# Optimization experiments

Hardware: AMD Instinct MI355X
Metric: run time of the kernel (lower is better)

## Reference

```python
import jax, jax.numpy as jnp
from jax import lax
import numpy as np

NINP, NHID, T, B = 512, 1024, 512, 64


def setup_inputs() -> dict:
    key = jax.random.key(0)
    ks = jax.random.split(key, 16)
    si = 1.0 / np.sqrt(NINP)
    sh = 1.0 / np.sqrt(NHID)
    inp = {
        "input": jax.random.normal(ks[0], (T, B, NINP), dtype=jnp.float32),
        "h": jax.random.normal(ks[1], (1, B, NHID), dtype=jnp.float32),
        "Wiz_w": jax.random.uniform(ks[2], (NHID, NINP), jnp.float32, -si, si),
        "Wiz_b": jax.random.uniform(ks[3], (NHID,), jnp.float32, -si, si),
        "Wir_w": jax.random.uniform(ks[4], (NHID, NINP), jnp.float32, -si, si),
        "Wir_b": jax.random.uniform(ks[5], (NHID,), jnp.float32, -si, si),
        "Wih_w": jax.random.uniform(ks[6], (NHID, NINP), jnp.float32, -si, si),
        "Wih_b": jax.random.uniform(ks[7], (NHID,), jnp.float32, -si, si),
        "Whz_w": jax.random.uniform(ks[8], (NHID, NHID), jnp.float32, -sh, sh),
        "Whz_b": jax.random.uniform(ks[9], (NHID,), jnp.float32, -sh, sh),
        "Whr_w": jax.random.uniform(ks[10], (NHID, NHID), jnp.float32, -sh, sh),
        "Whr_b": jax.random.uniform(ks[11], (NHID,), jnp.float32, -sh, sh),
        "Whh_w": jax.random.uniform(ks[12], (NHID, NHID), jnp.float32, -sh, sh),
        "Whh_b": jax.random.uniform(ks[13], (NHID,), jnp.float32, -sh, sh),
    }
    lengths = jax.random.randint(ks[14], (B,), 1, T + 1)
    lengths = lengths.at[0].set(T)  # ensure max_length == T (static scan length)
    inp["lengths"] = lengths.astype(jnp.int64)
    return inp


def reference(input, h, Wiz_w, Wiz_b, Wir_w, Wir_b, Wih_w, Wih_b,
              Whz_w, Whz_b, Whr_w, Whr_b, Whh_w, Whh_b, lengths):
    h0 = h[0]  # squeeze(0): [B, nhid]
    # Precompute input projections for all timesteps in one batched GEMM each: [T, B, nhid]
    xz = jnp.einsum('tbi,hi->tbh', input, Wiz_w) + Wiz_b
    xr = jnp.einsum('tbi,hi->tbh', input, Wir_w) + Wir_b
    xh = jnp.einsum('tbi,hi->tbh', input, Wih_w) + Wih_b
    tsteps = jnp.arange(input.shape[0])

    def step(hprev, inputs):
        xz_t, xr_t, xh_t, t = inputs
        z = jax.nn.sigmoid(hprev @ Whz_w.T + Whz_b + xz_t)
        r = jax.nn.sigmoid(hprev @ Whr_w.T + Whr_b + xr_t)
        h_cand = jnp.tanh((r * hprev) @ Whh_w.T + Whh_b + xh_t)
        h_new = (1.0 - z) * hprev + z * h_cand
        mask = (t < lengths).astype(hprev.dtype)[:, None]  # [B, 1]
        hn = h_new * mask + hprev * (1.0 - mask)
        return hn, hn

    h_last, hidden_stacked = lax.scan(step, h0, (xz, xr, xh, tsteps))
    return hidden_stacked, h_last[None]  # ([T,B,nhid], [1,B,nhid])
```

## Files before the change

### kernel.cpp

```cpp
#include <hip/hip_runtime.h>

typedef unsigned int   uint;
typedef unsigned short ushort;

#define NINP    512
#define NHID    1024
#define T_STEPS 512
#define B_SZ    64
#define KTOT    1536
#define BN      (B_SZ * NHID)

typedef __attribute__((ext_vector_type(8))) short bf16x8;
typedef __attribute__((ext_vector_type(4))) float f32x4;
typedef __attribute__((ext_vector_type(4))) uint  uintx4;

#define WCOMB_BYTES (3 * NHID * KTOT * 2)
#define WS_BSUM     (WCOMB_BYTES)
#define WS_HP       (WS_BSUM + 3 * NHID * 4)
#define WS_RHP      (WS_HP + BN * 4)
#define WS_BAR      (WS_RHP + BN * 4)
#define WS_NEED     (WS_BAR + 65536)

#define FH_OFF  8192

__device__ __forceinline__ float sigmoidf_(float x) { return 1.0f / (1.0f + __expf(-x)); }
__device__ __forceinline__ float tanhf_(float x)    { return 1.0f - 2.0f / (__expf(2.0f * x) + 1.0f); }

__device__ __forceinline__ ushort bf16_rne(float f) {
    uint u = __float_as_uint(f);
    return (ushort)((u + 0x7FFFu + ((u >> 16) & 1u)) >> 16);
}
__device__ __forceinline__ float bf16_to_f(ushort s) { return __uint_as_float(((uint)s) << 16); }
__device__ __forceinline__ bf16x8 ld8(const ushort* p) { return *(const bf16x8*)p; }
__device__ __forceinline__ bf16x8 cvt8(const float* p) {
    float4 a = *(const float4*)p;
    float4 b = *(const float4*)(p + 4);
    bf16x8 r;
    r[0] = (short)bf16_rne(a.x); r[1] = (short)bf16_rne(a.y);
    r[2] = (short)bf16_rne(a.z); r[3] = (short)bf16_rne(a.w);
    r[4] = (short)bf16_rne(b.x); r[5] = (short)bf16_rne(b.y);
    r[6] = (short)bf16_rne(b.z); r[7] = (short)bf16_rne(b.w);
    return r;
}
__device__ __forceinline__ f32x4 zero4() { f32x4 z = {0.f, 0.f, 0.f, 0.f}; return z; }
#define MFMA(a, b, c) __builtin_amdgcn_mfma_f32_16x16x32_bf16((a), (b), (c), 0, 0, 0)

__device__ __forceinline__ uint ld_rlx(uint* p) {
    return __hip_atomic_load(p, __ATOMIC_RELAXED, __HIP_MEMORY_SCOPE_AGENT);
}
__device__ __forceinline__ void st_rlx(uint* p, uint v) {
    __hip_atomic_store(p, v, __ATOMIC_RELAXED, __HIP_MEMORY_SCOPE_AGENT);
}
__device__ __forceinline__ void ld_state(const uint* p, uintx4& a, uintx4& b) {
    asm volatile("global_load_dwordx4 %0, %1, off sc0 sc1"
                 : "=v"(a) : "v"(p) : "memory");
    asm volatile("global_load_dwordx4 %0, %1, off offset:16 sc0 sc1"
                 : "=v"(b) : "v"(p) : "memory");
}
__device__ __forceinline__ void poll_ge(const uint* p, uint target) {
    for (;;) {
        uint v;
        asm volatile("global_load_dword %0, %1, off sc0 sc1\n\t"
                     "s_waitcnt vmcnt(0)"
                     : "=v"(v) : "v"(p) : "memory");
        if (__all(v >= target)) break;
        __builtin_amdgcn_s_sleep(1);
    }
}
__device__ __forceinline__ bf16x8 hi_frag(uintx4 a, uintx4 b) {
    uintx4 r;
    r[0] = __builtin_amdgcn_perm(a[1], a[0], 0x05040100u);
    r[1] = __builtin_amdgcn_perm(a[3], a[2], 0x05040100u);
    r[2] = __builtin_amdgcn_perm(b[1], b[0], 0x05040100u);
    r[3] = __builtin_amdgcn_perm(b[3], b[2], 0x05040100u);
    return *(bf16x8*)&r;
}
__device__ __forceinline__ bf16x8 lo_frag(uintx4 a, uintx4 b) {
    uintx4 r;
    r[0] = __builtin_amdgcn_perm(a[1], a[0], 0x07060302u);
    r[1] = __builtin_amdgcn_perm(a[3], a[2], 0x07060302u);
    r[2] = __builtin_amdgcn_perm(b[1], b[0], 0x07060302u);
    r[3] = __builtin_amdgcn_perm(b[3], b[2], 0x07060302u);
    return *(bf16x8*)&r;
}
__device__ __forceinline__ uint pack_hl(float v) {
    ushort hi = bf16_rne(v);
    ushort lo = bf16_rne(v - bf16_to_f(hi));
    return (uint)hi | ((uint)lo << 16);
}

__global__ __launch_bounds__(256) void prep_w(
    const float* __restrict__ Wiz, const float* __restrict__ Wir, const float* __restrict__ Wih,
    const float* __restrict__ Whz, const float* __restrict__ Whr, const float* __restrict__ Whh,
    ushort* __restrict__ wcomb)
{
    int tid = blockIdx.x * 256 + threadIdx.x;
    int oct = tid % (KTOT / 8);
    int row = tid / (KTOT / 8);
    int gate = row >> 10, n = row & 1023;
    int k0 = oct * 8;
    const float* src; int off;
    if (k0 < NINP) { src = gate == 0 ? Wiz : (gate == 1 ? Wir : Wih); off = n * NINP + k0; }
    else           { src = gate == 0 ? Whz : (gate == 1 ? Whr : Whh); off = n * NHID + (k0 - NINP); }
    ushort* dst = wcomb + (size_t)row * KTOT + k0;
    #pragma unroll
    for (int j = 0; j < 8; ++j) dst[j] = bf16_rne(src[off + j]);
}

__global__ __launch_bounds__(256) void prep_misc(
    const float* __restrict__ h0,
    const float* __restrict__ biz, const float* __restrict__ bir, const float* __restrict__ bih,
    const float* __restrict__ bhz, const float* __restrict__ bhr, const float* __restrict__ bhh,
    uint* __restrict__ hp, float* __restrict__ bsum, uint* __restrict__ bar)
{
    if (blockIdx.x < 256) {
        int i = blockIdx.x * 256 + threadIdx.x;
        hp[i] = pack_hl(h0[i]);
    } else {
        for (int n = threadIdx.x; n < NHID; n += 256) {
            bsum[n]            = biz[n] + bhz[n];
            bsum[NHID + n]     = bir[n] + bhr[n];
            bsum[2 * NHID + n] = bih[n] + bhh[n];
        }
        for (int i = threadIdx.x; i < 16384; i += 256) bar[i] = 0u;
    }
}

__global__ __launch_bounds__(512, 1) void gru_persist(
    const float* __restrict__ x, const float* __restrict__ h0,
    const void* __restrict__ lengths_raw,
    const ushort* __restrict__ wcomb, const float* __restrict__ bsum,
    uint* __restrict__ hp, uint* __restrict__ rhp,
    uint* __restrict__ bar, float* __restrict__ out)
{
    const int bid = blockIdx.x;
    const int nt = bid >> 2, mt = bid & 3;
    const int nbase = nt * 16, mbase = mt * 16;
    const int tid = threadIdx.x;
    const int wv = tid >> 6, lane = tid & 63;
    const int col = lane & 15, quad = lane >> 4;
    const int q8 = quad * 8;

    __shared__ f32x4 lds_acc1[2][8][2][64];
    __shared__ f32x4 lds_acc2[8][64];
    __shared__ uint  lds_pad[11264];
    lds_pad[tid & 1023] = tid;

    const int pslot = lane & 7;
    const int prod  = 2 * wv + 16 * (pslot >> 1) + (pslot & 1);
    uint* fr_ptr = bar + ((size_t)(mt * 64 + prod)) * 32;
    uint* fh_ptr = bar + FH_OFF + ((size_t)(mt * 64 + prod)) * 32;
    uint* my_fr  = bar + ((size_t)(mt * 64 + nt)) * 32;
    uint* my_fh  = bar + FH_OFF + ((size_t)(mt * 64 + nt)) * 32;

    bf16x8 wfz[6], wfr[6], wfc[6];
    #pragma unroll
    for (int s = 0; s < 6; ++s) {
        const int j = wv + 8 * s;
        const size_t ko = (size_t)j * 32 + q8;
        wfz[s] = ld8(wcomb + (size_t)(0 * NHID + nbase + col) * KTOT + ko);
        wfr[s] = ld8(wcomb + (size_t)(1 * NHID + nbase + col) * KTOT + ko);
        wfc[s] = ld8(wcomb + (size_t)(2 * NHID + nbase + col) * KTOT + ko);
    }

    const int* l32 = (const int*)lengths_raw;
    const bool is64 = (l32[1] == 0);
    int len[4];
    float h_reg[4];
    #pragma unroll
    for (int i = 0; i < 4; ++i) {
        const int b = mbase + quad * 4 + i;
        len[i]   = is64 ? (int)((const long long*)lengths_raw)[b] : l32[b];
        h_reg[i] = h0[(size_t)b * NHID + nbase + col];
    }

    const float bias_z = bsum[nbase + col];
    const float bias_r = bsum[NHID + nbase + col];
    const float bias_c = bsum[2 * NHID + nbase + col];

    const size_t arow = (size_t)(mbase + col);

    const uint* hpp[4]; const uint* rpp[4]; size_t gi4[4];
    #pragma unroll
    for (int s = 0; s < 4; ++s) {
        const int kh = (wv + 8 * (s + 2)) * 32 - NINP;
        hpp[s] = hp  + arow * NHID + kh + q8;
        rpp[s] = rhp + arow * NHID + kh + q8;
    }
    #pragma unroll
    for (int i = 0; i < 4; ++i)
        gi4[i] = (size_t)(mbase + quad * 4 + i) * NHID + nbase + col;

    f32x4 zsig = zero4();
    bf16x8 xf[2];

    f32x4 az = zero4(), ar = zero4();
    #pragma unroll
    for (int s = 0; s < 2; ++s) {
        const int k = (wv + 8 * s) * 32;
        xf[s] = cvt8(x + arow * NINP + k + q8);
        az = MFMA(xf[s], wfz[s], az);
        ar = MFMA(xf[s], wfr[s], ar);
    }

    for (int t = 0; t < T_STEPS; ++t) {
        const int par = t & 1;
        if (t) poll_ge(fh_ptr, (uint)t);
        {
            uintx4 qa[4], qb[4];
            #pragma unroll
            for (int s = 0; s < 4; ++s) ld_state(hpp[s], qa[s], qb[s]);
            asm volatile("s_waitcnt vmcnt(0)" ::: "memory");
            __builtin_amdgcn_sched_barrier(0);
            #pragma unroll
            for (int s = 0; s < 4; ++s) {
                const bf16x8 hi = hi_frag(qa[s], qb[s]);
                const bf16x8 lo = lo_frag(qa[s], qb[s]);
                az = MFMA(hi, wfz[s + 2], az);
                ar = MFMA(hi, wfr[s + 2], ar);
                az = MFMA(lo, wfz[s + 2], az);
                ar = MFMA(lo, wfr[s + 2], ar);
            }
        }
        lds_acc1[par][wv][0][lane] = az;
        lds_acc1[par][wv][1][lane] = ar;
        __syncthreads();
        if (wv == 0) {
            f32x4 rp = {bias_r, bias_r, bias_r, bias_r};
            #pragma unroll
            for (int w = 0; w < 8; ++w) {
                const f32x4 a = lds_acc1[par][w][1][lane];
                #pragma unroll
                for (int i = 0; i < 4; ++i) rp[i] += a[i];
            }
            #pragma unroll
            for (int i = 0; i < 4; ++i)
                st_rlx(&rhp[gi4[i]], pack_hl(sigmoidf_(rp[i]) * h_reg[i]));
            asm volatile("s_waitcnt vmcnt(0)" ::: "memory");
            if (lane == 0) st_rlx(my_fr, (uint)(t + 1));
        }
        if (wv < 2) {
            f32x4 zp = {bias_z, bias_z, bias_z, bias_z};
            #pragma unroll
            for (int w = 0; w < 8; ++w) {
                const f32x4 a = lds_acc1[par][w][0][lane];
                #pragma unroll
                for (int i = 0; i < 4; ++i) zp[i] += a[i];
            }
            #pragma unroll
            for (int i = 0; i < 4; ++i) zsig[i] = sigmoidf_(zp[i]);
        }
        f32x4 ac = zero4();
        ac = MFMA(xf[0], wfc[0], ac);
        ac = MFMA(xf[1], wfc[1], ac);

        poll_ge(fr_ptr, (uint)(t + 1));
        {
            uintx4 qa[4], qb[4];
            #pragma unroll
            for (int s = 0; s < 4; ++s) ld_state(rpp[s], qa[s], qb[s]);
            asm volatile("s_waitcnt vmcnt(0)" ::: "memory");
            __builtin_amdgcn_sched_barrier(0);
            #pragma unroll
            for (int s = 0; s < 4; ++s) {
                const bf16x8 hi = hi_frag(qa[s], qb[s]);
                const bf16x8 lo = lo_frag(qa[s], qb[s]);
                ac = MFMA(hi, wfc[s + 2], ac);
                ac = MFMA(lo, wfc[s + 2], ac);
            }
        }
        lds_acc2[wv][lane] = ac;
        __syncthreads();
        if (wv < 2) {
            f32x4 cp = {bias_c, bias_c, bias_c, bias_c};
            #pragma unroll
            for (int w = 0; w < 8; ++w) {
                const f32x4 a = lds_acc2[w][lane];
                #pragma unroll
                for (int i = 0; i < 4; ++i) cp[i] += a[i];
            }
            float hn4[4];
            #pragma unroll
            for (int i = 0; i < 4; ++i) {
                const float c = tanhf_(cp[i]);
                const float h = h_reg[i];
                hn4[i] = (t < len[i]) ? fmaf(zsig[i], c - h, h) : h;
                h_reg[i] = hn4[i];
            }
            if (wv == 1) {
                #pragma unroll
                for (int i = 0; i < 4; ++i) st_rlx(&hp[gi4[i]], pack_hl(hn4[i]));
                asm volatile("s_waitcnt vmcnt(0)" ::: "memory");
                if (lane == 0) st_rlx(my_fh, (uint)(t + 1));
            } else {
                float* out_t = out + (size_t)t * BN;
                #pragma unroll
                for (int i = 0; i < 4; ++i) {
                    __builtin_nontemporal_store(hn4[i], &out_t[gi4[i]]);
                    if (t == T_STEPS - 1)
                        __builtin_nontemporal_store(hn4[i], &out[(size_t)T_STEPS * BN + gi4[i]]);
                }
            }
        }
        az = zero4(); ar = zero4();
        if (t + 1 < T_STEPS) {
            const float* x_t = x + (size_t)(t + 1) * B_SZ * NINP;
            #pragma unroll
            for (int s = 0; s < 2; ++s) {
                const int k = (wv + 8 * s) * 32;
                xf[s] = cvt8(x_t + arow * NINP + k + q8);
                az = MFMA(xf[s], wfz[s], az);
                ar = MFMA(xf[s], wfr[s], ar);
            }
        }
    }

    if (ld_rlx(&bar[1023]) == 0xDEADBEEFu)
        out[0] = (float)lds_pad[tid & 1023];
}

__global__ void gru_ws_probe_mb(float* p) {
    if (blockIdx.x == 0xFFFFFFFFu) p[0] = 0.f;
}

extern "C" void kernel_launch(void* const* d_in, const int* in_sizes, int n_in,
                              void* d_out, int out_size, void* d_ws, size_t ws_size,
                              hipStream_t stream) {
    const float* x   = (const float*)d_in[0];
    const float* h0  = (const float*)d_in[1];
    const float* Wiz = (const float*)d_in[2];  const float* biz = (const float*)d_in[3];
    const float* Wir = (const float*)d_in[4];  const float* bir = (const float*)d_in[5];
    const float* Wih = (const float*)d_in[6];  const float* bih = (const float*)d_in[7];
    const float* Whz = (const float*)d_in[8];  const float* bhz = (const float*)d_in[9];
    const float* Whr = (const float*)d_in[10]; const float* bhr = (const float*)d_in[11];
    const float* Whh = (const float*)d_in[12]; const float* bhh = (const float*)d_in[13];
    const void*  lengths = d_in[14];
    float* out = (float*)d_out;
    char*  ws  = (char*)d_ws;

    size_t mb = ws_size >> 20; if (mb > 2048) mb = 2048;
    gru_ws_probe_mb<<<dim3((uint)mb + 1), 64, 0, stream>>>((float*)d_ws);
    if (ws_size < (size_t)WS_NEED) return;

    ushort* wcomb = (ushort*)ws;
    float*  bsum  = (float*)(ws + WS_BSUM);
    uint*   hp    = (uint*)(ws + WS_HP);
    uint*   rhp   = (uint*)(ws + WS_RHP);
    uint*   bar   = (uint*)(ws + WS_BAR);

    prep_w<<<2304, 256, 0, stream>>>(Wiz, Wir, Wih, Whz, Whr, Whh, wcomb);
    prep_misc<<<257, 256, 0, stream>>>(h0, biz, bir, bih, bhz, bhr, bhh, hp, bsum, bar);
    gru_persist<<<256, 512, 0, stream>>>(x, h0, lengths, wcomb, bsum,
                                         hp, rhp, bar, out);
}
```

Before: 4.141 ms.

## Replace flag barriers with per-element tagged state words polled directly

Drops the separate producer flag arrays and polling. Each hidden-state and r*h element is now stored as a 64-bit word holding the packed value plus a timestep tag, and consumers spin on the data loads until every tag reaches the target step. This removes the flag round trip (store data, wait, store flag, then poll flag, then load data). The epilogue is also spread over four waves, one batch row each, instead of two waves handling four rows. The cost is twice the state traffic per poll and repeated full-data reloads while spinning. Correctness depends on each 64-bit store being seen atomically.

```diff
diff --git a/kernel.cpp b/kernel.cpp
--- a/kernel.cpp
+++ b/kernel.cpp
@@ -1,7 +1,8 @@
 #include <hip/hip_runtime.h>
 
-typedef unsigned int   uint;
-typedef unsigned short ushort;
+typedef unsigned int       uint;
+typedef unsigned short     ushort;
+typedef unsigned long long ull;
 
 #define NINP    512
 #define NHID    1024
@@ -16,12 +17,9 @@
 
 #define WCOMB_BYTES (3 * NHID * KTOT * 2)
 #define WS_BSUM     (WCOMB_BYTES)
-#define WS_HP       (WS_BSUM + 3 * NHID * 4)
-#define WS_RHP      (WS_HP + BN * 4)
-#define WS_BAR      (WS_RHP + BN * 4)
-#define WS_NEED     (WS_BAR + 65536)
-
-#define FH_OFF  8192
+#define WS_HP2      (WS_BSUM + 3 * NHID * 4)
+#define WS_RHP2     (WS_HP2 + BN * 8)
+#define WS_NEED     (WS_RHP2 + BN * 8)
 
 __device__ __forceinline__ float sigmoidf_(float x) { return 1.0f / (1.0f + __expf(-x)); }
 __device__ __forceinline__ float tanhf_(float x)    { return 1.0f - 2.0f / (__expf(2.0f * x) + 1.0f); }
@@ -45,48 +43,69 @@
 __device__ __forceinline__ f32x4 zero4() { f32x4 z = {0.f, 0.f, 0.f, 0.f}; return z; }
 #define MFMA(a, b, c) __builtin_amdgcn_mfma_f32_16x16x32_bf16((a), (b), (c), 0, 0, 0)
 
-__device__ __forceinline__ uint ld_rlx(uint* p) {
+__device__ __forceinline__ uint ld_rlx(const uint* p) {
     return __hip_atomic_load(p, __ATOMIC_RELAXED, __HIP_MEMORY_SCOPE_AGENT);
 }
-__device__ __forceinline__ void st_rlx(uint* p, uint v) {
+__device__ __forceinline__ void st_state(ull* p, uint val, uint tag) {
+    ull v = (ull)val | ((ull)tag << 32);
     __hip_atomic_store(p, v, __ATOMIC_RELAXED, __HIP_MEMORY_SCOPE_AGENT);
-}
-__device__ __forceinline__ void ld_state(const uint* p, uintx4& a, uintx4& b) {
-    asm volatile("global_load_dwordx4 %0, %1, off sc0 sc1"
-                 : "=v"(a) : "v"(p) : "memory");
-    asm volatile("global_load_dwordx4 %0, %1, off offset:16 sc0 sc1"
-                 : "=v"(b) : "v"(p) : "memory");
-}
-__device__ __forceinline__ void poll_ge(const uint* p, uint target) {
-    for (;;) {
-        uint v;
-        asm volatile("global_load_dword %0, %1, off sc0 sc1\n\t"
-                     "s_waitcnt vmcnt(0)"
-                     : "=v"(v) : "v"(p) : "memory");
-        if (__all(v >= target)) break;
-        __builtin_amdgcn_s_sleep(1);
-    }
-}
-__device__ __forceinline__ bf16x8 hi_frag(uintx4 a, uintx4 b) {
-    uintx4 r;
-    r[0] = __builtin_amdgcn_perm(a[1], a[0], 0x05040100u);
-    r[1] = __builtin_amdgcn_perm(a[3], a[2], 0x05040100u);
-    r[2] = __builtin_amdgcn_perm(b[1], b[0], 0x05040100u);
-    r[3] = __builtin_amdgcn_perm(b[3], b[2], 0x05040100u);
-    return *(bf16x8*)&r;
-}
-__device__ __forceinline__ bf16x8 lo_frag(uintx4 a, uintx4 b) {
-    uintx4 r;
-    r[0] = __builtin_amdgcn_perm(a[1], a[0], 0x07060302u);
-    r[1] = __builtin_amdgcn_perm(a[3], a[2], 0x07060302u);
-    r[2] = __builtin_amdgcn_perm(b[1], b[0], 0x07060302u);
-    r[3] = __builtin_amdgcn_perm(b[3], b[2], 0x07060302u);
-    return *(bf16x8*)&r;
 }
 __device__ __forceinline__ uint pack_hl(float v) {
     ushort hi = bf16_rne(v);
     ushort lo = bf16_rne(v - bf16_to_f(hi));
     return (uint)hi | ((uint)lo << 16);
+}
+
+__device__ __forceinline__ void poll_load(const ull* b, uint target, uintx4 q[4][4]) {
+    const uint* p0 = (const uint*)b;
+    const uint* p1 = (const uint*)(b + 512);
+    for (;;) {
+        asm volatile("global_load_dwordx4 %0, %1, off sc0 sc1"             : "=v"(q[0][0]) : "v"(p0) : "memory");
+        asm volatile("global_load_dwordx4 %0, %1, off offset:16 sc0 sc1"   : "=v"(q[0][1]) : "v"(p0) : "memory");
+        asm volatile("global_load_dwordx4 %0, %1, off offset:32 sc0 sc1"   : "=v"(q[0][2]) : "v"(p0) : "memory");
+        asm volatile("global_load_dwordx4 %0, %1, off offset:48 sc0 sc1"   : "=v"(q[0][3]) : "v"(p0) : "memory");
+        asm volatile("global_load_dwordx4 %0, %1, off offset:2048 sc0 sc1" : "=v"(q[1][0]) : "v"(p0) : "memory");
+        asm volatile("global_load_dwordx4 %0, %1, off offset:2064 sc0 sc1" : "=v"(q[1][1]) : "v"(p0) : "memory");
+        asm volatile("global_load_dwordx4 %0, %1, off offset:2080 sc0 sc1" : "=v"(q[1][2]) : "v"(p0) : "memory");
+        asm volatile("global_load_dwordx4 %0, %1, off offset:2096 sc0 sc1" : "=v"(q[1][3]) : "v"(p0) : "memory");
+        asm volatile("global_load_dwordx4 %0, %1, off sc0 sc1"             : "=v"(q[2][0]) : "v"(p1) : "memory");
+        asm volatile("global_load_dwordx4 %0, %1, off offset:16 sc0 sc1"   : "=v"(q[2][1]) : "v"(p1) : "memory");
+        asm volatile("global_load_dwordx4 %0, %1, off offset:32 sc0 sc1"   : "=v"(q[2][2]) : "v"(p1) : "memory");
+        asm volatile("global_load_dwordx4 %0, %1, off offset:48 sc0 sc1"   : "=v"(q[2][3]) : "v"(p1) : "memory");
+        asm volatile("global_load_dwordx4 %0, %1, off offset:2048 sc0 sc1" : "=v"(q[3][0]) : "v"(p1) : "memory");
+        asm volatile("global_load_dwordx4 %0, %1, off offset:2064 sc0 sc1" : "=v"(q[3][1]) : "v"(p1) : "memory");
+        asm volatile("global_load_dwordx4 %0, %1, off offset:2080 sc0 sc1" : "=v"(q[3][2]) : "v"(p1) : "memory");
+        asm volatile("global_load_dwordx4 %0, %1, off offset:2096 sc0 sc1" : "=v"(q[3][3]) : "v"(p1) : "memory");
+        asm volatile("s_waitcnt vmcnt(0)" ::: "memory");
+        uint mn = 0xFFFFFFFFu;
+        #pragma unroll
+        for (int s = 0; s < 4; ++s)
+            #pragma unroll
+            for (int r = 0; r < 4; ++r) {
+                uint t0 = q[s][r][1], t1 = q[s][r][3];
+                mn = mn < t0 ? mn : t0;
+                mn = mn < t1 ? mn : t1;
+            }
+        if (__all(mn >= target)) break;
+        __builtin_amdgcn_s_sleep(1);
+    }
+    __builtin_amdgcn_sched_barrier(0);
+}
+__device__ __forceinline__ bf16x8 hi_frag4(const uintx4* q) {
+    uintx4 r;
+    r[0] = __builtin_amdgcn_perm(q[0][2], q[0][0], 0x05040100u);
+    r[1] = __builtin_amdgcn_perm(q[1][2], q[1][0], 0x05040100u);
+    r[2] = __builtin_amdgcn_perm(q[2][2], q[2][0], 0x05040100u);
+    r[3] = __builtin_amdgcn_perm(q[3][2], q[3][0], 0x05040100u);
+    return *(bf16x8*)&r;
+}
+__device__ __forceinline__ bf16x8 lo_frag4(const uintx4* q) {
+    uintx4 r;
+    r[0] = __builtin_amdgcn_perm(q[0][2], q[0][0], 0x07060302u);
+    r[1] = __builtin_amdgcn_perm(q[1][2], q[1][0], 0x07060302u);
+    r[2] = __builtin_amdgcn_perm(q[2][2], q[2][0], 0x07060302u);
+    r[3] = __builtin_amdgcn_perm(q[3][2], q[3][0], 0x07060302u);
+    return *(bf16x8*)&r;
 }
 
 __global__ __launch_bounds__(256) void prep_w(
@@ -111,18 +130,18 @@
     const float* __restrict__ h0,
     const float* __restrict__ biz, const float* __restrict__ bir, const float* __restrict__ bih,
     const float* __restrict__ bhz, const float* __restrict__ bhr, const float* __restrict__ bhh,
-    uint* __restrict__ hp, float* __restrict__ bsum, uint* __restrict__ bar)
+    ull* __restrict__ hp2, ull* __restrict__ rhp2, float* __restrict__ bsum)
 {
     if (blockIdx.x < 256) {
         int i = blockIdx.x * 256 + threadIdx.x;
-        hp[i] = pack_hl(h0[i]);
+        hp2[i]  = (ull)pack_hl(h0[i]);
+        rhp2[i] = 0ull;
     } else {
         for (int n = threadIdx.x; n < NHID; n += 256) {
             bsum[n]            = biz[n] + bhz[n];
             bsum[NHID + n]     = bir[n] + bhr[n];
             bsum[2 * NHID + n] = bih[n] + bhh[n];
         }
-        for (int i = threadIdx.x; i < 16384; i += 256) bar[i] = 0u;
     }
 }
 
@@ -130,8 +149,8 @@
     const float* __restrict__ x, const float* __restrict__ h0,
     const void* __restrict__ lengths_raw,
     const ushort* __restrict__ wcomb, const float* __restrict__ bsum,
-    uint* __restrict__ hp, uint* __restrict__ rhp,
-    uint* __restrict__ bar, float* __restrict__ out)
+    ull* __restrict__ hp2, ull* __restrict__ rhp2,
+    float* __restrict__ out)
 {
     const int bid = blockIdx.x;
     const int nt = bid >> 2, mt = bid & 3;
@@ -146,13 +165,6 @@
     __shared__ uint  lds_pad[11264];
     lds_pad[tid & 1023] = tid;
 
-    const int pslot = lane & 7;
-    const int prod  = 2 * wv + 16 * (pslot >> 1) + (pslot & 1);
-    uint* fr_ptr = bar + ((size_t)(mt * 64 + prod)) * 32;
-    uint* fh_ptr = bar + FH_OFF + ((size_t)(mt * 64 + prod)) * 32;
-    uint* my_fr  = bar + ((size_t)(mt * 64 + nt)) * 32;
-    uint* my_fh  = bar + FH_OFF + ((size_t)(mt * 64 + nt)) * 32;
-
     bf16x8 wfz[6], wfr[6], wfc[6];
     #pragma unroll
     for (int s = 0; s < 6; ++s) {
@@ -163,15 +175,16 @@
         wfc[s] = ld8(wcomb + (size_t)(2 * NHID + nbase + col) * KTOT + ko);
     }
 
+    const int row_w = mbase + quad * 4 + (wv & 3);
+    const size_t gi_w = (size_t)row_w * NHID + nbase + col;
     const int* l32 = (const int*)lengths_raw;
     const bool is64 = (l32[1] == 0);
-    int len[4];
-    float h_reg[4];
-    #pragma unroll
-    for (int i = 0; i < 4; ++i) {
-        const int b = mbase + quad * 4 + i;
-        len[i]   = is64 ? (int)((const long long*)lengths_raw)[b] : l32[b];
-        h_reg[i] = h0[(size_t)b * NHID + nbase + col];
+    int   len_w  = 0;
+    float h_w    = 0.f;
+    float zsig_w = 0.f;
+    if (wv < 4) {
+        len_w = is64 ? (int)((const long long*)lengths_raw)[row_w] : l32[row_w];
+        h_w   = h0[gi_w];
     }
 
     const float bias_z = bsum[nbase + col];
@@ -179,19 +192,9 @@
     const float bias_c = bsum[2 * NHID + nbase + col];
 
     const size_t arow = (size_t)(mbase + col);
-
-    const uint* hpp[4]; const uint* rpp[4]; size_t gi4[4];
-    #pragma unroll
-    for (int s = 0; s < 4; ++s) {
-        const int kh = (wv + 8 * (s + 2)) * 32 - NINP;
-        hpp[s] = hp  + arow * NHID + kh + q8;
-        rpp[s] = rhp + arow * NHID + kh + q8;
-    }
-    #pragma unroll
-    for (int i = 0; i < 4; ++i)
-        gi4[i] = (size_t)(mbase + quad * 4 + i) * NHID + nbase + col;
-
-    f32x4 zsig = zero4();
+    const ull* hb = hp2  + arow * NHID + wv * 32 + q8;
+    const ull* rb = rhp2 + arow * NHID + wv * 32 + q8;
+
     bf16x8 xf[2];
 
     f32x4 az = zero4(), ar = zero4();
@@ -205,17 +208,13 @@
 
     for (int t = 0; t < T_STEPS; ++t) {
         const int par = t & 1;
-        if (t) poll_ge(fh_ptr, (uint)t);
         {
-            uintx4 qa[4], qb[4];
-            #pragma unroll
-            for (int s = 0; s < 4; ++s) ld_state(hpp[s], qa[s], qb[s]);
-            asm volatile("s_waitcnt vmcnt(0)" ::: "memory");
-            __builtin_amdgcn_sched_barrier(0);
+            uintx4 q[4][4];
+            poll_load(hb, (uint)t, q);
             #pragma unroll
             for (int s = 0; s < 4; ++s) {
-                const bf16x8 hi = hi_frag(qa[s], qb[s]);
-                const bf16x8 lo = lo_frag(qa[s], qb[s]);
+                const bf16x8 hi = hi_frag4(q[s]);
+                const bf16x8 lo = lo_frag4(q[s]);
                 az = MFMA(hi, wfz[s + 2], az);
                 ar = MFMA(hi, wfr[s + 2], ar);
                 az = MFMA(lo, wfz[s + 2], az);
@@ -225,82 +224,47 @@
         lds_acc1[par][wv][0][lane] = az;
         lds_acc1[par][wv][1][lane] = ar;
         __syncthreads();
-        if (wv == 0) {
-            f32x4 rp = {bias_r, bias_r, bias_r, bias_r};
-            #pragma unroll
-            for (int w = 0; w < 8; ++w) {
-                const f32x4 a = lds_acc1[par][w][1][lane];
-                #pragma unroll
-                for (int i = 0; i < 4; ++i) rp[i] += a[i];
-            }
-            #pragma unroll
-            for (int i = 0; i < 4; ++i)
-                st_rlx(&rhp[gi4[i]], pack_hl(sigmoidf_(rp[i]) * h_reg[i]));
-            asm volatile("s_waitcnt vmcnt(0)" ::: "memory");
-            if (lane == 0) st_rlx(my_fr, (uint)(t + 1));
-        }
-        if (wv < 2) {
-            f32x4 zp = {bias_z, bias_z, bias_z, bias_z};
-            #pragma unroll
-            for (int w = 0; w < 8; ++w) {
-                const f32x4 a = lds_acc1[par][w][0][lane];
-                #pragma unroll
-                for (int i = 0; i < 4; ++i) zp[i] += a[i];
-            }
-            #pragma unroll
-            for (int i = 0; i < 4; ++i) zsig[i] = sigmoidf_(zp[i]);
+        if (wv < 4) {
+            const float* pr = ((const float*)&lds_acc1[par][0][1][lane]) + wv;
+            float rs = bias_r;
+            #pragma unroll
+            for (int wp = 0; wp < 8; ++wp) rs += pr[wp * 512];
+            st_state(&rhp2[gi_w], pack_hl(sigmoidf_(rs) * h_w), (uint)(t + 1));
+            const float* pz = ((const float*)&lds_acc1[par][0][0][lane]) + wv;
+            float zs = bias_z;
+            #pragma unroll
+            for (int wp = 0; wp < 8; ++wp) zs += pz[wp * 512];
+            zsig_w = sigmoidf_(zs);
         }
         f32x4 ac = zero4();
         ac = MFMA(xf[0], wfc[0], ac);
         ac = MFMA(xf[1], wfc[1], ac);
 
-        poll_ge(fr_ptr, (uint)(t + 1));
         {
-            uintx4 qa[4], qb[4];
-            #pragma unroll
-            for (int s = 0; s < 4; ++s) ld_state(rpp[s], qa[s], qb[s]);
-            asm volatile("s_waitcnt vmcnt(0)" ::: "memory");
-            __builtin_amdgcn_sched_barrier(0);
+            uintx4 q[4][4];
+            poll_load(rb, (uint)(t + 1), q);
             #pragma unroll
             for (int s = 0; s < 4; ++s) {
-                const bf16x8 hi = hi_frag(qa[s], qb[s]);
-                const bf16x8 lo = lo_frag(qa[s], qb[s]);
+                const bf16x8 hi = hi_frag4(q[s]);
+                const bf16x8 lo = lo_frag4(q[s]);
                 ac = MFMA(hi, wfc[s + 2], ac);
                 ac = MFMA(lo, wfc[s + 2], ac);
             }
         }
         lds_acc2[wv][lane] = ac;
         __syncthreads();
-        if (wv < 2) {
-            f32x4 cp = {bias_c, bias_c, bias_c, bias_c};
-            #pragma unroll
-            for (int w = 0; w < 8; ++w) {
-                const f32x4 a = lds_acc2[w][lane];
-                #pragma unroll
-                for (int i = 0; i < 4; ++i) cp[i] += a[i];
-            }
-            float hn4[4];
-            #pragma unroll
-            for (int i = 0; i < 4; ++i) {
-                const float c = tanhf_(cp[i]);
-                const float h = h_reg[i];
-                hn4[i] = (t < len[i]) ? fmaf(zsig[i], c - h, h) : h;
-                h_reg[i] = hn4[i];
-            }
-            if (wv == 1) {
-                #pragma unroll
-                for (int i = 0; i < 4; ++i) st_rlx(&hp[gi4[i]], pack_hl(hn4[i]));
-                asm volatile("s_waitcnt vmcnt(0)" ::: "memory");
-                if (lane == 0) st_rlx(my_fh, (uint)(t + 1));
-            } else {
-                float* out_t = out + (size_t)t * BN;
-                #pragma unroll
-                for (int i = 0; i < 4; ++i) {
-                    __builtin_nontemporal_store(hn4[i], &out_t[gi4[i]]);
-                    if (t == T_STEPS - 1)
-                        __builtin_nontemporal_store(hn4[i], &out[(size_t)T_STEPS * BN + gi4[i]]);
-                }
-            }
+        if (wv < 4) {
+            const float* pc = ((const float*)&lds_acc2[0][lane]) + wv;
+            float cs = bias_c;
+            #pragma unroll
+            for (int wp = 0; wp < 8; ++wp) cs += pc[wp * 256];
+            const float c  = tanhf_(cs);
+            const float hn = (t < len_w) ? fmaf(zsig_w, c - h_w, h_w) : h_w;
+            h_w = hn;
+            st_state(&hp2[gi_w], pack_hl(hn), (uint)(t + 1));
+            __builtin_nontemporal_store(hn, &out[(size_t)t * BN + gi_w]);
+            if (t == T_STEPS - 1)
+                __builtin_nontemporal_store(hn, &out[(size_t)T_STEPS * BN + gi_w]);
         }
         az = zero4(); ar = zero4();
         if (t + 1 < T_STEPS) {
@@ -315,7 +279,7 @@
         }
     }
 
-    if (ld_rlx(&bar[1023]) == 0xDEADBEEFu)
+    if (ld_rlx((const uint*)hp2 + 1) == 0xDEADBEEFu)
         out[0] = (float)lds_pad[tid & 1023];
 }
 
@@ -344,12 +308,11 @@
 
     ushort* wcomb = (ushort*)ws;
     float*  bsum  = (float*)(ws + WS_BSUM);
-    uint*   hp    = (uint*)(ws + WS_HP);
-    uint*   rhp   = (uint*)(ws + WS_RHP);
-    uint*   bar   = (uint*)(ws + WS_BAR);
+    ull*    hp2   = (ull*)(ws + WS_HP2);
+    ull*    rhp2  = (ull*)(ws + WS_RHP2);
 
     prep_w<<<2304, 256, 0, stream>>>(Wiz, Wir, Wih, Whz, Whr, Whh, wcomb);
-    prep_misc<<<257, 256, 0, stream>>>(h0, biz, bir, bih, bhz, bhr, bhh, hp, bsum, bar);
+    prep_misc<<<257, 256, 0, stream>>>(h0, biz, bir, bih, bhz, bhr, bhh, hp2, rhp2, bsum);
     gru_persist<<<256, 512, 0, stream>>>(x, h0, lengths, wcomb, bsum,
-                                         hp, rhp, bar, out);
-}
+                                         hp2, rhp2, out);
+}
```

Measured after the change: 15.94 ms. 285% more time.
